# Optimization experiments

Measured on AMD Instinct MI355X. Metric: run time of the kernel, lower is better.

Reference implementation:

```python
import jax, jax.numpy as jnp
import numpy as np

H, D = 8, 16            # num_heads, head_size
IN = H * D              # hgt_in_dim = 128
NT, ET = 3, 4           # node types, edge types (hard-coded in module)
N_DRUG, N_DIS, N_PROT = 10000, 10000, 30000
N = N_DRUG + N_DIS + N_PROT
E = 400000
LAYERS = 2
SQRT_D = float(np.sqrt(D))

# homogeneous node-type vector (presorted by type, as dgl.to_homogeneous yields)
NTYPE = jnp.concatenate([
    jnp.zeros(N_DRUG, jnp.int32),
    jnp.ones(N_DIS, jnp.int32),
    jnp.full((N_PROT,), 2, jnp.int32),
])


def typed_linear(x, types, W):
    # x: (M, in), W: (T, in, out), types: (M,) -> y[m] = x[m] @ W[types[m]]
    out = jnp.zeros((x.shape[0], W.shape[2]), x.dtype)
    for t in range(W.shape[0]):
        out = out + jnp.where((types == t)[:, None], x @ W[t], 0.0)
    return out


def hgt_conv(x, src, dst, etype, Wk, Wq, Wv, Wa, rel_att, rel_msg, pri, skip):
    # type-specific K/Q/V projections
    k = typed_linear(x, NTYPE, Wk).reshape(N, H, D)
    q = typed_linear(x, NTYPE, Wq).reshape(N, H, D)
    v = typed_linear(x, NTYPE, Wv).reshape(N, H, D)
    ke, qe, ve = k[src], q[dst], v[src]          # (E, H, D) gathers

    # per-edge-type relation transforms (vectorized over heads)
    kw = jnp.zeros_like(ke)
    mw = jnp.zeros_like(ve)
    for t in range(ET):
        sel = (etype == t)[:, None, None]
        kw = kw + jnp.where(sel, jnp.einsum('ehd,hdo->eho', ke, rel_att[:, t]), 0.0)
        mw = mw + jnp.where(sel, jnp.einsum('ehd,hdo->eho', ve, rel_msg[:, t]), 0.0)

    # attention logits: (kw . q) * relation_pri[head, etype] / sqrt(D)
    a = (kw * qe).sum(-1) * pri.T[etype] / SQRT_D  # (E, H)

    # edge softmax grouped by destination node, per head
    amax = jax.ops.segment_max(a, dst, num_segments=N)      # (N, H)
    ea = jnp.exp(a - amax[dst])
    esum = jax.ops.segment_sum(ea, dst, num_segments=N)
    attn = ea / esum[dst]                                   # (E, H)

    # weighted message aggregation (scatter-add over dst)
    m = mw * attn[..., None]                                 # (E, H, D)
    h = jax.ops.segment_sum(m, dst, num_segments=N).reshape(N, IN)

    # output projection (dropout = identity in eval) + sigmoid-skip residual
    h = typed_linear(h, NTYPE, Wa)
    alpha = jax.nn.sigmoid(skip)[NTYPE][:, None]
    return h * alpha + x * (1.0 - alpha)


def setup_inputs() -> dict:
    key = jax.random.key(0)
    ks = jax.random.split(key, 12)
    s = 0.05
    return {
        "drug_feature": jax.random.normal(ks[0], (N_DRUG, IN), jnp.float32),
        "disease_feature": jax.random.normal(ks[1], (N_DIS, IN), jnp.float32),
        "protein_feature": jax.random.normal(ks[2], (N_PROT, IN), jnp.float32),
        "src": jax.random.randint(ks[3], (E,), 0, N, dtype=jnp.int32),
        "dst": jax.random.randint(ks[4], (E,), 0, N, dtype=jnp.int32),
        "etype": jnp.sort(jax.random.randint(ks[5], (E,), 0, ET, dtype=jnp.int32)),
        "Wk": jax.random.normal(ks[6], (NT, IN, IN), jnp.float32) * s,
        "Wq": jax.random.normal(ks[7], (NT, IN, IN), jnp.float32) * s,
        "Wv": jax.random.normal(ks[8], (NT, IN, IN), jnp.float32) * s,
        "Wa": jax.random.normal(ks[9], (NT, IN, IN), jnp.float32) * s,
        "rel_att": jax.random.normal(ks[10], (H, ET, D, D), jnp.float32) * 0.1,
        "rel_msg": jax.random.normal(ks[11], (H, ET, D, D), jnp.float32) * 0.1,
        "pri": jnp.ones((H, ET), jnp.float32),
        "skip": jnp.ones((NT,), jnp.float32),
    }


def reference(drug_feature, disease_feature, protein_feature, src, dst, etype,
              Wk, Wq, Wv, Wa, rel_att, rel_msg, pri, skip):
    x = jnp.concatenate([drug_feature, disease_feature, protein_feature], axis=0)
    # ModuleList holds the SAME conv instance -> shared weights across layers
    for _ in range(LAYERS):
        x = hgt_conv(x, src, dst, etype, Wk, Wq, Wv, Wa, rel_att, rel_msg, pri, skip)
    return x
```

## Files before the change

### kernel.cpp

```cpp
#include <hip/hip_runtime.h>

#define N_NODE 50000
#define N_EDGE 400000
#define INF    128

#define FUSED_BLOCKS 1024

#define MT0 157
#define MT1 157
#define MT2 469
#define MTILES 783

typedef __bf16 bf16x8 __attribute__((ext_vector_type(8)));
typedef float  f32x4  __attribute__((ext_vector_type(4)));

__device__ __forceinline__ void seg_decode64(int b, int& ty, int& base, int& nrows) {
  if (b < MT0)          { ty = 0; base = b * 64;                nrows = 10000 - base; }
  else if (b < MT0+MT1) { ty = 1; base = 10000 + (b - MT0)*64;  nrows = 20000 - base; }
  else                  { ty = 2; base = 20000 + (b-MT0-MT1)*64; nrows = 50000 - base; }
  if (nrows > 64) nrows = 64;
}

__device__ __forceinline__ float blo(unsigned u) { return __uint_as_float(u << 16); }
__device__ __forceinline__ float bhi(unsigned u) { return __uint_as_float(u & 0xffff0000u); }
__device__ __forceinline__ unsigned bpack(float lo, float hi) {
  unsigned a = __float_as_uint(lo), b = __float_as_uint(hi);
  a = (a + 0x7fffu + ((a >> 16) & 1u)) >> 16;
  b = (b + 0x7fffu + ((b >> 16) & 1u)) & 0xffff0000u;
  return a | b;
}
__device__ __forceinline__ unsigned short b16(float v) {
  unsigned u = __float_as_uint(v);
  return (unsigned short)((u + 0x7fffu + ((u >> 16) & 1u)) >> 16);
}
__device__ __forceinline__ bf16x8 ld_frag(const unsigned short* p) {
  uint4 u = *reinterpret_cast<const uint4*>(p);
  return __builtin_bit_cast(bf16x8, u);
}
__device__ __forceinline__ float dot4(float4 a, float4 b) {
  return a.x*b.x + a.y*b.y + a.z*b.z + a.w*b.w;
}

__global__ __launch_bounds__(256) void k_concat(const float* __restrict__ dr,
                                                const float* __restrict__ di,
                                                const float* __restrict__ pr,
                                                float* __restrict__ x,
                                                unsigned short* __restrict__ xh) {
  for (int i = blockIdx.x * 256 + threadIdx.x; i < N_NODE * 32; i += 2048 * 256) {
    int row = i >> 5;
    float4 val;
    if (row < 10000)      val = ((const float4*)dr)[i];
    else if (row < 20000) val = ((const float4*)di)[i - 10000*32];
    else                  val = ((const float4*)pr)[i - 20000*32];
    ((float4*)x)[i] = val;
    ((uint2*)xh)[i] = make_uint2(bpack(val.x, val.y), bpack(val.z, val.w));
  }
}

__global__ __launch_bounds__(256) void k_count(const int* __restrict__ dst, int* __restrict__ deg) {
  int e = blockIdx.x * 256 + threadIdx.x;
  if (e < N_EDGE) atomicAdd(&deg[dst[e]], 1);
}

__global__ __launch_bounds__(1024) void k_scan(const int* __restrict__ deg,
                                               int* __restrict__ off, int* __restrict__ cur) {
  __shared__ int part[1024];
  int t = threadIdx.x;
  int c0 = t * 49;
  int c1 = c0 + 49; if (c1 > N_NODE) c1 = N_NODE;
  int s = 0;
  for (int i = c0; i < c1; ++i) s += deg[i];
  part[t] = s;
  __syncthreads();
  for (int ofs = 1; ofs < 1024; ofs <<= 1) {
    int v = (t >= ofs) ? part[t - ofs] : 0;
    __syncthreads();
    part[t] += v;
    __syncthreads();
  }
  int run = (t == 0) ? 0 : part[t - 1];
  for (int i = c0; i < c1; ++i) { off[i] = run; cur[i] = run; run += deg[i]; }
  if (t == 1023) off[N_NODE] = part[1023];
}

__global__ __launch_bounds__(256) void k_fill(const int* __restrict__ dst,
                                              const int* __restrict__ src,
                                              const int* __restrict__ etp,
                                              int* __restrict__ cur, int* __restrict__ est) {
  int e = blockIdx.x * 256 + threadIdx.x;
  if (e < N_EDGE) {
    int p = atomicAdd(&cur[dst[e]], 1);
    est[p] = (src[e] << 2) | etp[e];
  }
}

__global__ __launch_bounds__(256) void k_trmsg(const float* __restrict__ rm,
                                               float* __restrict__ AmT) {
  int i = blockIdx.x * 256 + threadIdx.x;
  int di = i & 15, doo = (i >> 4) & 15, ty = (i >> 8) & 3, hh = i >> 10;
  AmT[i] = rm[((hh * 4 + ty) * 16 + di) * 16 + doo];
}

__global__ __launch_bounds__(256) void k_twt(const float* __restrict__ Wk,
                                             const float* __restrict__ Wq,
                                             const float* __restrict__ Wv,
                                             const float* __restrict__ Wa,
                                             unsigned short* __restrict__ WT) {
  int idx = blockIdx.x * 256 + threadIdx.x;
  if (idx >= 196608) return;
  int mt = idx >> 14;
  int within = idx & 16383;
  int o = within >> 7, ii = within & 127;
  int mat = mt / 3, ty = mt % 3;
  const float* W = (mat == 0) ? Wk : (mat == 1) ? Wq : (mat == 2) ? Wv : Wa;
  WT[idx] = b16(W[ty * 16384 + ii * 128 + o]);
}

__global__ __launch_bounds__(256) void k_qkv(const unsigned short* __restrict__ xh,
                                             const unsigned short* __restrict__ WT,
                                             const float* __restrict__ rel_att,
                                             const float* __restrict__ pri,
                                             uint2* __restrict__ kvb,
                                             uint4* __restrict__ qab) {
  __shared__ float qs[4][16][128];
  int ty, base, nrows;
  seg_decode64(blockIdx.x, ty, base, nrows);
  int w = threadIdx.x >> 6, l = threadIdx.x & 63;
  int r16 = l & 15, ks = l >> 4;
  int row0 = base + w * 16;
  int wrows = nrows - w * 16;

  bf16x8 a[4];
  const unsigned short* xrow = xh + (size_t)(row0 + r16) * 128 + ks * 8;
#pragma unroll
  for (int kk = 0; kk < 4; ++kk) a[kk] = ld_frag(xrow + kk * 32);

  const unsigned short* WK = WT + (size_t)(0 * 3 + ty) * 16384;
  const unsigned short* WQ = WT + (size_t)(1 * 3 + ty) * 16384;
  const unsigned short* WV = WT + (size_t)(2 * 3 + ty) * 16384;

#pragma unroll 1
  for (int ct = 0; ct < 8; ++ct) {
    int o = ct * 16 + r16;
    const unsigned short* bk = WK + (size_t)o * 128 + ks * 8;
    const unsigned short* bq = WQ + (size_t)o * 128 + ks * 8;
    const unsigned short* bv = WV + (size_t)o * 128 + ks * 8;
    f32x4 ak = {0.f,0.f,0.f,0.f}, aq = {0.f,0.f,0.f,0.f}, av = {0.f,0.f,0.f,0.f};
#pragma unroll
    for (int kk = 0; kk < 4; ++kk) {
      bf16x8 fbk = ld_frag(bk + kk * 32);
      bf16x8 fbq = ld_frag(bq + kk * 32);
      bf16x8 fbv = ld_frag(bv + kk * 32);
      ak = __builtin_amdgcn_mfma_f32_16x16x32_bf16(a[kk], fbk, ak, 0, 0, 0);
      aq = __builtin_amdgcn_mfma_f32_16x16x32_bf16(a[kk], fbq, aq, 0, 0, 0);
      av = __builtin_amdgcn_mfma_f32_16x16x32_bf16(a[kk], fbv, av, 0, 0, 0);
    }
#pragma unroll
    for (int r = 0; r < 4; ++r) {
      int rrel = ks * 4 + r;
      float kn = __shfl_xor(ak[r], 1);
      float vn = __shfl_xor(av[r], 1);
      qs[w][rrel][o] = aq[r];
      if (rrel < wrows && (l & 1) == 0) {
        size_t p = (size_t)(row0 + rrel);
        kvb[p * 64 + (o >> 1)] = make_uint2(bpack(ak[r], kn), bpack(av[r], vn));
      }
    }
  }

  int h = l >> 3, j = l & 7;
  float4 prh = ((const float4*)pri)[h];
  float prs[4] = { prh.x * 0.25f, prh.y * 0.25f, prh.z * 0.25f, prh.w * 0.25f };
  int lim = wrows < 16 ? (wrows < 0 ? 0 : wrows) : 16;
  for (int nd = 0; nd < lim; ++nd) {
    float4 q0 = *(float4*)&qs[w][nd][h * 16 + 0];
    float4 q1 = *(float4*)&qs[w][nd][h * 16 + 4];
    float4 q2 = *(float4*)&qs[w][nd][h * 16 + 8];
    float4 q3 = *(float4*)&qs[w][nd][h * 16 + 12];
    unsigned pk[4];
#pragma unroll
    for (int t4 = 0; t4 < 4; ++t4) {
      const float4* Ar = (const float4*)(rel_att + (((h * 4 + t4) * 16) + 2 * j) * 16);
      float ax = dot4(Ar[0], q0) + dot4(Ar[1], q1) + dot4(Ar[2], q2) + dot4(Ar[3], q3);
      float ay = dot4(Ar[4], q0) + dot4(Ar[5], q1) + dot4(Ar[6], q2) + dot4(Ar[7], q3);
      pk[t4] = bpack(ax * prs[t4], ay * prs[t4]);
    }
    qab[(size_t)(row0 + nd) * 64 + l] = make_uint4(pk[0], pk[1], pk[2], pk[3]);
  }
}

__global__ __launch_bounds__(256)
__attribute__((amdgpu_waves_per_eu(4, 4)))
void k_fused(const uint2* __restrict__ kvb,
             const uint4* __restrict__ qab,
             const int* __restrict__ off,
             const int* __restrict__ est,
             const float* __restrict__ AmT,
             unsigned* __restrict__ hbh) {
  __shared__ float accs[4][4][128];
  int w = threadIdx.x >> 6, l = threadIdx.x & 63;
  int h = l >> 3, j = l & 7;

  for (int n = blockIdx.x * 4 + w; n < N_NODE; n += FUSED_BLOCKS * 4) {
    int o0 = off[n], o1 = off[n + 1];

    uint4 qu = qab[(size_t)n * 64 + l];
    float2 qa0 = make_float2(blo(qu.x), bhi(qu.x));
    float2 qa1 = make_float2(blo(qu.y), bhi(qu.y));
    float2 qa2 = make_float2(blo(qu.z), bhi(qu.z));
    float2 qa3 = make_float2(blo(qu.w), bhi(qu.w));

    float ssum = 0.f;
    float2 z = make_float2(0.f, 0.f);
    float2 at0 = z, at1 = z, at2 = z, at3 = z;

#define PROC(KV, TY, VALID) { \
    int ty = (TY) & 3; \
    float kx = blo((KV).x), ky = bhi((KV).x); \
    float2 qat = (ty==0)?qa0:(ty==1)?qa1:(ty==2)?qa2:qa3; \
    float part = kx*qat.x + ky*qat.y; \
    part += __shfl_xor(part, 1); \
    part += __shfl_xor(part, 2); \
    part += __shfl_xor(part, 4); \
    float wgt = (VALID) ? __expf(part) : 0.f; \
    ssum += wgt; \
    float vx = blo((KV).y), vy = bhi((KV).y); \
    float w0=(ty==0)?wgt:0.f, w1=(ty==1)?wgt:0.f, w2=(ty==2)?wgt:0.f, w3=(ty==3)?wgt:0.f; \
    at0.x += w0*vx; at0.y += w0*vy; \
    at1.x += w1*vx; at1.y += w1*vy; \
    at2.x += w2*vx; at2.y += w2*vy; \
    at3.x += w3*vx; at3.y += w3*vy; }

    for (int b0 = o0; b0 < o1; b0 += 64) {
      int cnt = o1 - b0; if (cnt > 64) cnt = 64;
      int stv = est[b0 + (l < cnt ? l : cnt - 1)];
      int t0 = __shfl(stv, 0);
      int t1 = __shfl(stv, 1 < cnt ? 1 : 0);
      uint2 kv0 = kvb[(size_t)(t0 >> 2) * 64 + l];
      uint2 kv1 = kvb[(size_t)(t1 >> 2) * 64 + l];
      for (int i = 0; i < cnt; i += 2) {
        bool more = (i + 2) < cnt;
        int n0 = 0, n1 = 0; uint2 kn0, kn1;
        if (more) {
          n0 = __shfl(stv, i + 2);
          n1 = __shfl(stv, (i + 3) < cnt ? (i + 3) : (i + 2));
          kn0 = kvb[(size_t)(n0 >> 2) * 64 + l];
          kn1 = kvb[(size_t)(n1 >> 2) * 64 + l];
        }
        PROC(kv0, t0, true)
        PROC(kv1, t1, (i + 1) < cnt)
        if (more) { t0 = n0; t1 = n1; kv0 = kn0; kv1 = kn1; }
      }
    }
#undef PROC

    float inv = (ssum > 0.f) ? 1.f / ssum : 0.f;
    at0.x *= inv; at0.y *= inv;
    at1.x *= inv; at1.y *= inv;
    at2.x *= inv; at2.y *= inv;
    at3.x *= inv; at3.y *= inv;

    ((float2*)&accs[w][0][0])[l] = at0;
    ((float2*)&accs[w][1][0])[l] = at1;
    ((float2*)&accs[w][2][0])[l] = at2;
    ((float2*)&accs[w][3][0])[l] = at3;

    float ox = 0.f, oy = 0.f;
#pragma unroll
    for (int ty = 0; ty < 4; ++ty) {
      const float4* AmR = (const float4*)(AmT + ((h * 4 + ty) * 16) * 16);
#pragma unroll
      for (int d4 = 0; d4 < 4; ++d4) {
        float4 ac = *((float4*)&accs[w][ty][h * 16 + d4 * 4]);
        float4 m0 = AmR[(2 * j) * 4 + d4];
        float4 m1 = AmR[(2 * j + 1) * 4 + d4];
        ox += m0.x * ac.x + m0.y * ac.y + m0.z * ac.z + m0.w * ac.w;
        oy += m1.x * ac.x + m1.y * ac.y + m1.z * ac.z + m1.w * ac.w;
      }
    }
    hbh[(size_t)n * 64 + l] = bpack(ox, oy);
  }
}

__global__ __launch_bounds__(256) void k_out(const unsigned short* __restrict__ hbh,
                                             const unsigned short* __restrict__ WT,
                                             const float* __restrict__ skipv,
                                             float* __restrict__ xio,
                                             unsigned short* __restrict__ xh,
                                             int write_xh) {
  int ty, base, nrows;
  seg_decode64(blockIdx.x, ty, base, nrows);
  int w = threadIdx.x >> 6, l = threadIdx.x & 63;
  int r16 = l & 15, ks = l >> 4;
  int row0 = base + w * 16;
  int wrows = nrows - w * 16;

  bf16x8 a[4];
  const unsigned short* hrow = hbh + (size_t)(row0 + r16) * 128 + ks * 8;
#pragma unroll
  for (int kk = 0; kk < 4; ++kk) a[kk] = ld_frag(hrow + kk * 32);

  const unsigned short* WA = WT + (size_t)(3 * 3 + ty) * 16384;
  float alpha = 1.f / (1.f + __expf(-skipv[ty]));
  float beta = 1.f - alpha;

#pragma unroll 1
  for (int ct = 0; ct < 8; ++ct) {
    int o = ct * 16 + r16;
    const unsigned short* ba = WA + (size_t)o * 128 + ks * 8;
    f32x4 acc = {0.f,0.f,0.f,0.f};
#pragma unroll
    for (int kk = 0; kk < 4; ++kk)
      acc = __builtin_amdgcn_mfma_f32_16x16x32_bf16(a[kk], ld_frag(ba + kk * 32), acc, 0, 0, 0);
#pragma unroll
    for (int r = 0; r < 4; ++r) {
      int rrel = ks * 4 + r;
      size_t p = (size_t)(row0 + rrel) * 128 + o;
      float nx = 0.f;
      if (rrel < wrows) {
        nx = acc[r] * alpha + xio[p] * beta;
        xio[p] = nx;
      }
      float nxn = __shfl_xor(nx, 1);
      if (write_xh && rrel < wrows && (l & 1) == 0)
        ((unsigned*)xh)[p >> 1] = bpack(nx, nxn);
    }
  }
}

extern "C" void kernel_launch(void* const* d_in, const int* in_sizes, int n_in,
                              void* d_out, int out_size, void* d_ws, size_t ws_size,
                              hipStream_t stream) {
  const float* drug = (const float*)d_in[0];
  const float* dis  = (const float*)d_in[1];
  const float* prot = (const float*)d_in[2];
  const int* src    = (const int*)d_in[3];
  const int* dst    = (const int*)d_in[4];
  const int* etp    = (const int*)d_in[5];
  const float* Wk   = (const float*)d_in[6];
  const float* Wq   = (const float*)d_in[7];
  const float* Wv   = (const float*)d_in[8];
  const float* Wa   = (const float*)d_in[9];
  const float* rel_att = (const float*)d_in[10];
  const float* rel_msg = (const float*)d_in[11];
  const float* pri  = (const float*)d_in[12];
  const float* skip = (const float*)d_in[13];
  float* x = (float*)d_out;

  char* w = (char*)d_ws;
  uint2*          kvb = (uint2*)(w + 0);
  unsigned*       hbh = (unsigned*)(w + 25600000);
  uint4*          qab = (uint4*)(w + 38400000);
  unsigned short* xh  = (unsigned short*)(w + 89600000);
  unsigned short* WT  = (unsigned short*)(w + 102400000);
  float*          AmT = (float*)(w + 102793216);
  int*            off = (int*)(w + 102825984);
  int*            est = (int*)(w + 103026048);
  int*            deg = (int*)(w + 25600000);
  int*            cur = (int*)(w + 25800064);

  k_concat<<<2048, 256, 0, stream>>>(drug, dis, prot, x, xh);

  (void)hipMemsetAsync(deg, 0, N_NODE * sizeof(int), stream);
  (void)hipMemsetAsync(est + N_EDGE, 0, 64 * sizeof(int), stream);
  k_count<<<(N_EDGE + 255) / 256, 256, 0, stream>>>(dst, deg);
  k_scan<<<1, 1024, 0, stream>>>(deg, off, cur);
  k_fill<<<(N_EDGE + 255) / 256, 256, 0, stream>>>(dst, src, etp, cur, est);

  k_trmsg<<<32, 256, 0, stream>>>(rel_msg, AmT);
  k_twt<<<768, 256, 0, stream>>>(Wk, Wq, Wv, Wa, WT);

  for (int layer = 0; layer < 2; ++layer) {
    k_qkv<<<MTILES, 256, 0, stream>>>(xh, WT, rel_att, pri, kvb, qab);
    k_fused<<<FUSED_BLOCKS, 256, 0, stream>>>(kvb, qab, off, est, AmT, hbh);
    k_out<<<MTILES, 256, 0, stream>>>((const unsigned short*)hbh, WT, skip, x, xh,
                                      layer == 0 ? 1 : 0);
  }
}
```

Before: 849.4 us.

## Process 32-row tiles per wave to reuse weight fragments across two MFMA subtiles

Each wave in the QKV and output projection kernels now handles 32 rows, loading weight fragments once and applying them to two 16-row subtiles, with blocks covering four independent tiles. The Q staging buffer in shared memory is stored as bf16 instead of fp32 to save LDS. This aims to cut redundant weight loads and launch count, at the cost of more registers per wave and slightly lower Q precision before the relation transform.

```diff
diff --git a/kernel.cpp b/kernel.cpp
--- a/kernel.cpp
+++ b/kernel.cpp
@@ -6,19 +6,20 @@
 
 #define FUSED_BLOCKS 1024
 
-#define MT0 157
-#define MT1 157
-#define MT2 469
-#define MTILES 783
+#define TILES0 313
+#define TILES1 313
+#define TILES2 938
+#define PTILES 1564
+#define PBLOCKS 391
 
 typedef __bf16 bf16x8 __attribute__((ext_vector_type(8)));
 typedef float  f32x4  __attribute__((ext_vector_type(4)));
 
-__device__ __forceinline__ void seg_decode64(int b, int& ty, int& base, int& nrows) {
-  if (b < MT0)          { ty = 0; base = b * 64;                nrows = 10000 - base; }
-  else if (b < MT0+MT1) { ty = 1; base = 10000 + (b - MT0)*64;  nrows = 20000 - base; }
-  else                  { ty = 2; base = 20000 + (b-MT0-MT1)*64; nrows = 50000 - base; }
-  if (nrows > 64) nrows = 64;
+__device__ __forceinline__ void seg_decode(int b, int& ty, int& base, int& nrows) {
+  if (b < TILES0)            { ty = 0; base = b * 32;                      nrows = 10000 - base; }
+  else if (b < TILES0+TILES1){ ty = 1; base = 10000 + (b - TILES0) * 32;   nrows = 20000 - base; }
+  else                       { ty = 2; base = 20000 + (b - TILES0-TILES1)*32; nrows = 50000 - base; }
+  if (nrows > 32) nrows = 32;
 }
 
 __device__ __forceinline__ float blo(unsigned u) { return __uint_as_float(u << 16); }
@@ -36,9 +37,6 @@
 __device__ __forceinline__ bf16x8 ld_frag(const unsigned short* p) {
   uint4 u = *reinterpret_cast<const uint4*>(p);
   return __builtin_bit_cast(bf16x8, u);
-}
-__device__ __forceinline__ float dot4(float4 a, float4 b) {
-  return a.x*b.x + a.y*b.y + a.z*b.z + a.w*b.w;
 }
 
 __global__ __launch_bounds__(256) void k_concat(const float* __restrict__ dr,
@@ -122,18 +120,21 @@
                                              const float* __restrict__ pri,
                                              uint2* __restrict__ kvb,
                                              uint4* __restrict__ qab) {
-  __shared__ float qs[4][16][128];
-  int ty, base, nrows;
-  seg_decode64(blockIdx.x, ty, base, nrows);
+  __shared__ unsigned short qsh[4][32][128];
   int w = threadIdx.x >> 6, l = threadIdx.x & 63;
   int r16 = l & 15, ks = l >> 4;
-  int row0 = base + w * 16;
-  int wrows = nrows - w * 16;
-
-  bf16x8 a[4];
-  const unsigned short* xrow = xh + (size_t)(row0 + r16) * 128 + ks * 8;
-#pragma unroll
-  for (int kk = 0; kk < 4; ++kk) a[kk] = ld_frag(xrow + kk * 32);
+  int tile = blockIdx.x * 4 + w;
+  int ty, base, wrows;
+  seg_decode(tile, ty, base, wrows);
+  int row0 = base;
+
+  bf16x8 a[2][4];
+#pragma unroll
+  for (int st = 0; st < 2; ++st) {
+    const unsigned short* xrow = xh + (size_t)(row0 + st * 16 + r16) * 128 + ks * 8;
+#pragma unroll
+    for (int kk = 0; kk < 4; ++kk) a[st][kk] = ld_frag(xrow + kk * 32);
+  }
 
   const unsigned short* WK = WT + (size_t)(0 * 3 + ty) * 16384;
   const unsigned short* WQ = WT + (size_t)(1 * 3 + ty) * 16384;
@@ -142,28 +143,32 @@
 #pragma unroll 1
   for (int ct = 0; ct < 8; ++ct) {
     int o = ct * 16 + r16;
-    const unsigned short* bk = WK + (size_t)o * 128 + ks * 8;
-    const unsigned short* bq = WQ + (size_t)o * 128 + ks * 8;
-    const unsigned short* bv = WV + (size_t)o * 128 + ks * 8;
-    f32x4 ak = {0.f,0.f,0.f,0.f}, aq = {0.f,0.f,0.f,0.f}, av = {0.f,0.f,0.f,0.f};
+    bf16x8 fbk[4], fbq[4], fbv[4];
 #pragma unroll
     for (int kk = 0; kk < 4; ++kk) {
-      bf16x8 fbk = ld_frag(bk + kk * 32);
-      bf16x8 fbq = ld_frag(bq + kk * 32);
-      bf16x8 fbv = ld_frag(bv + kk * 32);
-      ak = __builtin_amdgcn_mfma_f32_16x16x32_bf16(a[kk], fbk, ak, 0, 0, 0);
-      aq = __builtin_amdgcn_mfma_f32_16x16x32_bf16(a[kk], fbq, aq, 0, 0, 0);
-      av = __builtin_amdgcn_mfma_f32_16x16x32_bf16(a[kk], fbv, av, 0, 0, 0);
-    }
-#pragma unroll
-    for (int r = 0; r < 4; ++r) {
-      int rrel = ks * 4 + r;
-      float kn = __shfl_xor(ak[r], 1);
-      float vn = __shfl_xor(av[r], 1);
-      qs[w][rrel][o] = aq[r];
-      if (rrel < wrows && (l & 1) == 0) {
-        size_t p = (size_t)(row0 + rrel);
-        kvb[p * 64 + (o >> 1)] = make_uint2(bpack(ak[r], kn), bpack(av[r], vn));
+      fbk[kk] = ld_frag(WK + (size_t)o * 128 + ks * 8 + kk * 32);
+      fbq[kk] = ld_frag(WQ + (size_t)o * 128 + ks * 8 + kk * 32);
+      fbv[kk] = ld_frag(WV + (size_t)o * 128 + ks * 8 + kk * 32);
+    }
+#pragma unroll
+    for (int st = 0; st < 2; ++st) {
+      f32x4 ak = {0.f,0.f,0.f,0.f}, aq = {0.f,0.f,0.f,0.f}, av = {0.f,0.f,0.f,0.f};
+#pragma unroll
+      for (int kk = 0; kk < 4; ++kk) {
+        ak = __builtin_amdgcn_mfma_f32_16x16x32_bf16(a[st][kk], fbk[kk], ak, 0, 0, 0);
+        aq = __builtin_amdgcn_mfma_f32_16x16x32_bf16(a[st][kk], fbq[kk], aq, 0, 0, 0);
+        av = __builtin_amdgcn_mfma_f32_16x16x32_bf16(a[st][kk], fbv[kk], av, 0, 0, 0);
+      }
+#pragma unroll
+      for (int r = 0; r < 4; ++r) {
+        int rrel = st * 16 + ks * 4 + r;
+        float kn = __shfl_xor(ak[r], 1);
+        float vn = __shfl_xor(av[r], 1);
+        qsh[w][rrel][o] = b16(aq[r]);
+        if (rrel < wrows && (l & 1) == 0) {
+          size_t p = (size_t)(row0 + rrel);
+          kvb[p * 64 + (o >> 1)] = make_uint2(bpack(ak[r], kn), bpack(av[r], vn));
+        }
       }
     }
   }
@@ -171,18 +176,23 @@
   int h = l >> 3, j = l & 7;
   float4 prh = ((const float4*)pri)[h];
   float prs[4] = { prh.x * 0.25f, prh.y * 0.25f, prh.z * 0.25f, prh.w * 0.25f };
-  int lim = wrows < 16 ? (wrows < 0 ? 0 : wrows) : 16;
-  for (int nd = 0; nd < lim; ++nd) {
-    float4 q0 = *(float4*)&qs[w][nd][h * 16 + 0];
-    float4 q1 = *(float4*)&qs[w][nd][h * 16 + 4];
-    float4 q2 = *(float4*)&qs[w][nd][h * 16 + 8];
-    float4 q3 = *(float4*)&qs[w][nd][h * 16 + 12];
+  for (int nd = 0; nd < wrows; ++nd) {
+    unsigned u[8];
+    *(uint4*)&u[0] = *(uint4*)&qsh[w][nd][h * 16 + 0];
+    *(uint4*)&u[4] = *(uint4*)&qsh[w][nd][h * 16 + 8];
+    float qf[16];
+#pragma unroll
+    for (int q2 = 0; q2 < 8; ++q2) { qf[2*q2] = blo(u[q2]); qf[2*q2+1] = bhi(u[q2]); }
     unsigned pk[4];
 #pragma unroll
     for (int t4 = 0; t4 < 4; ++t4) {
-      const float4* Ar = (const float4*)(rel_att + (((h * 4 + t4) * 16) + 2 * j) * 16);
-      float ax = dot4(Ar[0], q0) + dot4(Ar[1], q1) + dot4(Ar[2], q2) + dot4(Ar[3], q3);
-      float ay = dot4(Ar[4], q0) + dot4(Ar[5], q1) + dot4(Ar[6], q2) + dot4(Ar[7], q3);
+      const float* Ar = rel_att + (((h * 4 + t4) * 16) + 2 * j) * 16;
+      float ax = 0.f, ay = 0.f;
+#pragma unroll
+      for (int o = 0; o < 16; ++o) {
+        ax += Ar[o] * qf[o];
+        ay += Ar[16 + o] * qf[o];
+      }
       pk[t4] = bpack(ax * prs[t4], ay * prs[t4]);
     }
     qab[(size_t)(row0 + nd) * 64 + l] = make_uint4(pk[0], pk[1], pk[2], pk[3]);
@@ -288,17 +298,20 @@
                                              float* __restrict__ xio,
                                              unsigned short* __restrict__ xh,
                                              int write_xh) {
-  int ty, base, nrows;
-  seg_decode64(blockIdx.x, ty, base, nrows);
   int w = threadIdx.x >> 6, l = threadIdx.x & 63;
   int r16 = l & 15, ks = l >> 4;
-  int row0 = base + w * 16;
-  int wrows = nrows - w * 16;
-
-  bf16x8 a[4];
-  const unsigned short* hrow = hbh + (size_t)(row0 + r16) * 128 + ks * 8;
-#pragma unroll
-  for (int kk = 0; kk < 4; ++kk) a[kk] = ld_frag(hrow + kk * 32);
+  int tile = blockIdx.x * 4 + w;
+  int ty, base, wrows;
+  seg_decode(tile, ty, base, wrows);
+  int row0 = base;
+
+  bf16x8 a[2][4];
+#pragma unroll
+  for (int st = 0; st < 2; ++st) {
+    const unsigned short* hrow = hbh + (size_t)(row0 + st * 16 + r16) * 128 + ks * 8;
+#pragma unroll
+    for (int kk = 0; kk < 4; ++kk) a[st][kk] = ld_frag(hrow + kk * 32);
+  }
 
   const unsigned short* WA = WT + (size_t)(3 * 3 + ty) * 16384;
   float alpha = 1.f / (1.f + __expf(-skipv[ty]));
@@ -307,23 +320,29 @@
 #pragma unroll 1
   for (int ct = 0; ct < 8; ++ct) {
     int o = ct * 16 + r16;
-    const unsigned short* ba = WA + (size_t)o * 128 + ks * 8;
-    f32x4 acc = {0.f,0.f,0.f,0.f};
+    bf16x8 ba[4];
 #pragma unroll
     for (int kk = 0; kk < 4; ++kk)
-      acc = __builtin_amdgcn_mfma_f32_16x16x32_bf16(a[kk], ld_frag(ba + kk * 32), acc, 0, 0, 0);
-#pragma unroll
-    for (int r = 0; r < 4; ++r) {
-      int rrel = ks * 4 + r;
-      size_t p = (size_t)(row0 + rrel) * 128 + o;
-      float nx = 0.f;
-      if (rrel < wrows) {
-        nx = acc[r] * alpha + xio[p] * beta;
-        xio[p] = nx;
-      }
-      float nxn = __shfl_xor(nx, 1);
-      if (write_xh && rrel < wrows && (l & 1) == 0)
-        ((unsigned*)xh)[p >> 1] = bpack(nx, nxn);
+      ba[kk] = ld_frag(WA + (size_t)o * 128 + ks * 8 + kk * 32);
+#pragma unroll
+    for (int st = 0; st < 2; ++st) {
+      f32x4 acc = {0.f,0.f,0.f,0.f};
+#pragma unroll
+      for (int kk = 0; kk < 4; ++kk)
+        acc = __builtin_amdgcn_mfma_f32_16x16x32_bf16(a[st][kk], ba[kk], acc, 0, 0, 0);
+#pragma unroll
+      for (int r = 0; r < 4; ++r) {
+        int rrel = st * 16 + ks * 4 + r;
+        size_t p = (size_t)(row0 + rrel) * 128 + o;
+        float nx = 0.f;
+        if (rrel < wrows) {
+          nx = acc[r] * alpha + xio[p] * beta;
+          xio[p] = nx;
+        }
+        float nxn = __shfl_xor(nx, 1);
+        if (write_xh && rrel < wrows && (l & 1) == 0)
+          ((unsigned*)xh)[p >> 1] = bpack(nx, nxn);
+      }
     }
   }
 }
@@ -371,9 +390,9 @@
   k_twt<<<768, 256, 0, stream>>>(Wk, Wq, Wv, Wa, WT);
 
   for (int layer = 0; layer < 2; ++layer) {
-    k_qkv<<<MTILES, 256, 0, stream>>>(xh, WT, rel_att, pri, kvb, qab);
+    k_qkv<<<PBLOCKS, 256, 0, stream>>>(xh, WT, rel_att, pri, kvb, qab);
     k_fused<<<FUSED_BLOCKS, 256, 0, stream>>>(kvb, qab, off, est, AmT, hbh);
-    k_out<<<MTILES, 256, 0, stream>>>((const unsigned short*)hbh, WT, skip, x, xh,
-                                      layer == 0 ? 1 : 0);
-  }
-}
+    k_out<<<PBLOCKS, 256, 0, stream>>>((const unsigned short*)hbh, WT, skip, x, xh,
+                                       layer == 0 ? 1 : 0);
+  }
+}
```

Result: faster. 795.5 us (-6.3%).
